# Kernel tuning notes

Measured on AMD Instinct MI355X. Metric: run time of the kernel, lower is better.

## Reference

```python
import jax, jax.numpy as jnp
import numpy as np

N, K, W = 500000, 512, 64


def setup_inputs() -> dict:
    key = jax.random.key(0)
    kx, kc = jax.random.split(key)
    X = jax.random.normal(kx, (N, W), dtype=jnp.float32)
    # nn.init.uniform_(codebook.weight, a=-1.0, b=1.0)
    codebook = jax.random.uniform(kc, (K, W), dtype=jnp.float32, minval=-1.0, maxval=1.0)
    return {"X": X, "codebook": codebook}


def reference(X, codebook):
    # torch.cdist (p=2): pairwise Euclidean distances [N, K]
    x2 = jnp.sum(X * X, axis=-1, keepdims=True)          # [N, 1]
    c2 = jnp.sum(codebook * codebook, axis=-1)           # [K]
    d2 = x2 - 2.0 * (X @ codebook.T) + c2[None, :]        # [N, K]
    dist = jnp.sqrt(jnp.maximum(d2, 0.0))
    idx = jnp.argmin(dist, axis=-1)                       # [N] int
    min_dists = jnp.min(dist, axis=-1)                    # [N] == gather(dist, idx)
    return idx, min_dists
```

## Files before the change

### kernel.cpp

```cpp
#include <hip/hip_runtime.h>

#define N_POINTS 500000
#define K_CENT   512
#define W_DIM    64
#define N_JOBS   (N_POINTS / 32)

typedef _Float16 half8 __attribute__((ext_vector_type(8)));
typedef float    f32x4 __attribute__((ext_vector_type(4)));

__global__ void cvt_kernel(const float* __restrict__ cb,
                           _Float16* __restrict__ cbf) {
    int id = blockIdx.x * 256 + threadIdx.x;
    if (id >= K_CENT * 8) return;
    int c = id >> 3, o = (id & 7) * 8;
    int t = c >> 5, csub = (c >> 4) & 1, r = c & 15;
    int kstep = o >> 5, grp = (o >> 3) & 3;
    int lane = grp * 16 + r;
    const float* src = cb + (size_t)c * W_DIM + o;
    half8 h, l;
#pragma unroll
    for (int j = 0; j < 8; ++j) {
        float w = -2.0f * src[j];
        _Float16 hh = (_Float16)w;
        h[j] = hh;
        l[j] = (_Float16)(w - (float)hh);
    }
    size_t bh = ((((size_t)t * 2 + 0) * 2 + csub) * 2 + kstep) * 512 + (size_t)lane * 8;
    size_t bl = ((((size_t)t * 2 + 1) * 2 + csub) * 2 + kstep) * 512 + (size_t)lane * 8;
    *(half8*)(cbf + bh) = h;
    *(half8*)(cbf + bl) = l;
}

__global__ void c2_kernel(const float* __restrict__ cb, float* __restrict__ c2) {
    int c = blockIdx.x * 256 + threadIdx.x;
    if (c >= K_CENT) return;
    const float4* row = (const float4*)(cb + (size_t)c * W_DIM);
    double s = 0.0;
#pragma unroll
    for (int j = 0; j < W_DIM / 4; ++j) {
        float4 v = row[j];
        s += (double)v.x * v.x + (double)v.y * v.y + (double)v.z * v.z + (double)v.w * v.w;
    }
    c2[c] = (float)s;
}

#define MFMA16(A, B, C) __builtin_amdgcn_mfma_f32_16x16x32_f16(A, B, C, 0, 0, 0)

#define STAGE(T, BUF)                                                          \
    {                                                                          \
        const __attribute__((address_space(1))) _Float16* g =                  \
            (const __attribute__((address_space(1))) _Float16*)                \
            (cbf + (size_t)(T) * 4096 + (size_t)wave * 1024 + (size_t)lane * 8); \
        __builtin_amdgcn_global_load_lds(                                      \
            (const __attribute__((address_space(1))) void*)g,                  \
            (__attribute__((address_space(3))) void*)&abuf[BUF][wave * 1024],  \
            16, 0, 0);                                                         \
        __builtin_amdgcn_global_load_lds(                                      \
            (const __attribute__((address_space(1))) void*)(g + 512),          \
            (__attribute__((address_space(3))) void*)&abuf[BUF][wave * 1024 + 512], \
            16, 0, 0);                                                         \
    }

#define MFMA_PHASE(BUF, ACC, Q0, Q1)                                           \
    {                                                                          \
        half8 aH[2][2], aL[2][2];                                              \
        _Pragma("unroll")                                                      \
        for (int cs = 0; cs < 2; ++cs)                                         \
            _Pragma("unroll")                                                  \
            for (int ks = 0; ks < 2; ++ks) {                                   \
                aH[cs][ks] = *(const half8*)&abuf[BUF][(cs * 2 + ks) * 512 + lane * 8]; \
                aL[cs][ks] = *(const half8*)&abuf[BUF][(4 + cs * 2 + ks) * 512 + lane * 8]; \
            }                                                                  \
        __builtin_amdgcn_s_setprio(1);                                         \
        _Pragma("unroll")                                                      \
        for (int cs = 0; cs < 2; ++cs)                                         \
            _Pragma("unroll")                                                  \
            for (int ps = 0; ps < 2; ++ps)                                     \
                ACC[cs][ps] = MFMA16(aH[cs][0], bh[ps][0], cs ? Q1 : Q0);      \
        _Pragma("unroll")                                                      \
        for (int cs = 0; cs < 2; ++cs)                                         \
            _Pragma("unroll")                                                  \
            for (int ps = 0; ps < 2; ++ps)                                     \
                ACC[cs][ps] = MFMA16(aH[cs][1], bh[ps][1], ACC[cs][ps]);       \
        _Pragma("unroll")                                                      \
        for (int cs = 0; cs < 2; ++cs)                                         \
            _Pragma("unroll")                                                  \
            for (int ps = 0; ps < 2; ++ps)                                     \
                ACC[cs][ps] = MFMA16(aL[cs][0], bh[ps][0], ACC[cs][ps]);       \
        _Pragma("unroll")                                                      \
        for (int cs = 0; cs < 2; ++cs)                                         \
            _Pragma("unroll")                                                  \
            for (int ps = 0; ps < 2; ++ps)                                     \
                ACC[cs][ps] = MFMA16(aL[cs][1], bh[ps][1], ACC[cs][ps]);       \
        _Pragma("unroll")                                                      \
        for (int cs = 0; cs < 2; ++cs)                                         \
            _Pragma("unroll")                                                  \
            for (int ps = 0; ps < 2; ++ps)                                     \
                ACC[cs][ps] = MFMA16(aH[cs][0], bl[ps][0], ACC[cs][ps]);       \
        _Pragma("unroll")                                                      \
        for (int cs = 0; cs < 2; ++cs)                                         \
            _Pragma("unroll")                                                  \
            for (int ps = 0; ps < 2; ++ps)                                     \
                ACC[cs][ps] = MFMA16(aH[cs][1], bl[ps][1], ACC[cs][ps]);       \
        __builtin_amdgcn_s_setprio(0);                                         \
    }

#define PAIR_ARGMIN(TA)                                                        \
    {                                                                          \
        _Pragma("unroll")                                                      \
        for (int ps = 0; ps < 2; ++ps) {                                       \
            float v0 = accP[0][ps][0], v1 = accP[0][ps][1];                    \
            float v2 = accP[0][ps][2], v3 = accP[0][ps][3];                    \
            float v4 = accP[1][ps][0], v5 = accP[1][ps][1];                    \
            float v6 = accP[1][ps][2], v7 = accP[1][ps][3];                    \
            float v8 = accQ[0][ps][0], v9 = accQ[0][ps][1];                    \
            float v10 = accQ[0][ps][2], v11 = accQ[0][ps][3];                  \
            float v12 = accQ[1][ps][0], v13 = accQ[1][ps][1];                  \
            float v14 = accQ[1][ps][2], v15 = accQ[1][ps][3];                  \
            float a0 = fminf(v0, v1),   a1 = fminf(v2, v3);                    \
            float a2 = fminf(v4, v5),   a3 = fminf(v6, v7);                    \
            float a4 = fminf(v8, v9),   a5 = fminf(v10, v11);                  \
            float a6 = fminf(v12, v13), a7 = fminf(v14, v15);                  \
            float b0 = fminf(a0, a1), b1 = fminf(a2, a3);                      \
            float b2 = fminf(a4, a5), b3 = fminf(a6, a7);                      \
            float c0 = fminf(b0, b1), c1 = fminf(b2, b3);                      \
            float m  = fminf(c0, c1);                                          \
            bool  L3 = (m == c0);                                              \
            float bL = L3 ? b0 : b2;                                           \
            bool  L2 = (m == bL);                                              \
            float aL = L3 ? (L2 ? a0 : a2) : (L2 ? a4 : a6);                   \
            bool  L1 = (m == aL);                                              \
            float vE = L3 ? (L2 ? (L1 ? v0 : v2) : (L1 ? v4 : v6))             \
                          : (L2 ? (L1 ? v8 : v10) : (L1 ? v12 : v14));         \
            bool  L0 = (m == vE);                                              \
            int ji = (L3 ? 0 : 8) | (L2 ? 0 : 4) | (L1 ? 0 : 2) | (L0 ? 0 : 1); \
            int jj = ji & 7;                                                   \
            int ci = ((TA) + (ji >> 3)) * 32 + (jj >> 2) * 16 + grp4 + (jj & 3); \
            bool imp = (m < bd[ps]) || (m == bd[ps] && ci < bi[ps]);           \
            bd[ps] = imp ? m : bd[ps];                                         \
            bi[ps] = imp ? ci : bi[ps];                                        \
        }                                                                      \
    }

__global__ __launch_bounds__(256, 2)
void kmeans_mfma(const float* __restrict__ X,
                 const _Float16* __restrict__ cbf,
                 const float* __restrict__ c2,
                 float* __restrict__ out_idx,
                 float* __restrict__ out_dist) {
    __shared__ _Float16 abuf[2][4096];
    __shared__ float c2s[K_CENT];
    int tid = threadIdx.x;
    c2s[tid] = c2[tid];
    c2s[tid + 256] = c2[tid + 256];

    int wave = tid >> 6;
    int lane = tid & 63;
    int l15  = lane & 15;
    int grp  = lane >> 4;
    int grp4 = grp * 4;
    int grp8 = grp * 8;
    int rot  = (blockIdx.x & 7) * 2;

    int job   = blockIdx.x * 4 + wave;
    int valid = job < N_JOBS;
    int jc    = valid ? job : (N_JOBS - 1);

    half8 bh[2][2], bl[2][2];
    float x2[2] = {0.f, 0.f};
#pragma unroll
    for (int ps = 0; ps < 2; ++ps) {
        int p = jc * 32 + ps * 16 + l15;
#pragma unroll
        for (int ks = 0; ks < 2; ++ks) {
            const float4* xp = (const float4*)(X + (size_t)p * W_DIM + ks * 32 + grp8);
            float4 f0 = xp[0], f1 = xp[1];
            float fa[8] = {f0.x, f0.y, f0.z, f0.w, f1.x, f1.y, f1.z, f1.w};
#pragma unroll
            for (int j = 0; j < 8; ++j) {
                _Float16 hh = (_Float16)fa[j];
                bh[ps][ks][j] = hh;
                bl[ps][ks][j] = (_Float16)(fa[j] - (float)hh);
                x2[ps] = fmaf(fa[j], fa[j], x2[ps]);
            }
        }
    }
#pragma unroll
    for (int ps = 0; ps < 2; ++ps) {
        x2[ps] += __shfl_xor(x2[ps], 16);
        x2[ps] += __shfl_xor(x2[ps], 32);
    }

    float bd[2] = {3.4e38f, 3.4e38f};
    int   bi[2] = {0, 0};
    f32x4 accP[2][2], accQ[2][2];

    STAGE(rot, 0)
    __syncthreads();

#pragma unroll 1
    for (int it = 0; it < 8; ++it) {
        int ta = (rot + 2 * it) & 15;
        f32x4 qa0 = *(const f32x4*)&c2s[ta * 32 + grp4];
        f32x4 qa1 = *(const f32x4*)&c2s[ta * 32 + 16 + grp4];
        f32x4 qb0 = *(const f32x4*)&c2s[ta * 32 + 32 + grp4];
        f32x4 qb1 = *(const f32x4*)&c2s[ta * 32 + 48 + grp4];
        STAGE(ta + 1, 1)
        MFMA_PHASE(0, accP, qa0, qa1)
        __syncthreads();
        if (it < 7) {
            int tn = (ta + 2) & 15;
            STAGE(tn, 0)
        }
        MFMA_PHASE(1, accQ, qb0, qb1)
        PAIR_ARGMIN(ta)
        __syncthreads();
    }

#pragma unroll
    for (int ps = 0; ps < 2; ++ps) {
        float od = __shfl_xor(bd[ps], 16); int oi = __shfl_xor(bi[ps], 16);
        if (od < bd[ps] || (od == bd[ps] && oi < bi[ps])) { bd[ps] = od; bi[ps] = oi; }
        od = __shfl_xor(bd[ps], 32); oi = __shfl_xor(bi[ps], 32);
        if (od < bd[ps] || (od == bd[ps] && oi < bi[ps])) { bd[ps] = od; bi[ps] = oi; }
    }

    if (valid && grp == 0) {
#pragma unroll
        for (int ps = 0; ps < 2; ++ps) {
            int p = jc * 32 + ps * 16 + l15;
            out_idx[p]  = (float)bi[ps];
            out_dist[p] = sqrtf(fmaxf(bd[ps] + x2[ps], 0.f));
        }
    }
}

extern "C" void kernel_launch(void* const* d_in, const int* in_sizes, int n_in,
                              void* d_out, int out_size, void* d_ws, size_t ws_size,
                              hipStream_t stream) {
    const float* X  = (const float*)d_in[0];
    const float* cb = (const float*)d_in[1];
    float* out      = (float*)d_out;

    _Float16* cbf = (_Float16*)d_ws;
    float*    c2  = (float*)(cbf + (size_t)K_CENT * W_DIM * 2);

    hipLaunchKernelGGL(cvt_kernel, dim3((K_CENT * 8 + 255) / 256), dim3(256), 0, stream, cb, cbf);
    hipLaunchKernelGGL(c2_kernel, dim3((K_CENT + 255) / 256), dim3(256), 0, stream, cb, c2);

    hipLaunchKernelGGL(kmeans_mfma, dim3((N_JOBS + 3) / 4), dim3(256), 0, stream,
                       X, cbf, c2, out, out + N_POINTS);
}
```

Before: 101.5 us.

## Process 64 points per wave to double codebook tile reuse

Each wave now handles 64 points (four 16-point groups) instead of 32, so every codebook tile staged in LDS is reused across twice as many MFMA columns. This halves the number of blocks and the total codebook staging and LDS reads per point. The argmin is done per 32-centroid chunk rather than per pair of chunks, and bounds guards handle the tail since 500000 is not divisible by 64. The cost is higher register pressure from the doubled accumulators and split-precision point fragments, which may reduce occupancy.

```diff
diff --git a/kernel.cpp b/kernel.cpp
--- a/kernel.cpp
+++ b/kernel.cpp
@@ -3,7 +3,7 @@
 #define N_POINTS 500000
 #define K_CENT   512
 #define W_DIM    64
-#define N_JOBS   (N_POINTS / 32)
+#define N_JOBS   ((N_POINTS + 63) / 64)
 
 typedef _Float16 half8 __attribute__((ext_vector_type(8)));
 typedef float    f32x4 __attribute__((ext_vector_type(4)));
@@ -61,7 +61,7 @@
             16, 0, 0);                                                         \
     }
 
-#define MFMA_PHASE(BUF, ACC, Q0, Q1)                                           \
+#define CHUNK_COMPUTE(BUF, T_)                                                 \
     {                                                                          \
         half8 aH[2][2], aL[2][2];                                              \
         _Pragma("unroll")                                                      \
@@ -71,71 +71,58 @@
                 aH[cs][ks] = *(const half8*)&abuf[BUF][(cs * 2 + ks) * 512 + lane * 8]; \
                 aL[cs][ks] = *(const half8*)&abuf[BUF][(4 + cs * 2 + ks) * 512 + lane * 8]; \
             }                                                                  \
+        f32x4 q0 = *(const f32x4*)&c2s[(T_) * 32 + grp4];                      \
+        f32x4 q1 = *(const f32x4*)&c2s[(T_) * 32 + 16 + grp4];                 \
+        f32x4 acc[2][4];                                                       \
         __builtin_amdgcn_s_setprio(1);                                         \
         _Pragma("unroll")                                                      \
         for (int cs = 0; cs < 2; ++cs)                                         \
             _Pragma("unroll")                                                  \
-            for (int ps = 0; ps < 2; ++ps)                                     \
-                ACC[cs][ps] = MFMA16(aH[cs][0], bh[ps][0], cs ? Q1 : Q0);      \
-        _Pragma("unroll")                                                      \
-        for (int cs = 0; cs < 2; ++cs)                                         \
-            _Pragma("unroll")                                                  \
-            for (int ps = 0; ps < 2; ++ps)                                     \
-                ACC[cs][ps] = MFMA16(aH[cs][1], bh[ps][1], ACC[cs][ps]);       \
-        _Pragma("unroll")                                                      \
-        for (int cs = 0; cs < 2; ++cs)                                         \
-            _Pragma("unroll")                                                  \
-            for (int ps = 0; ps < 2; ++ps)                                     \
-                ACC[cs][ps] = MFMA16(aL[cs][0], bh[ps][0], ACC[cs][ps]);       \
-        _Pragma("unroll")                                                      \
-        for (int cs = 0; cs < 2; ++cs)                                         \
-            _Pragma("unroll")                                                  \
-            for (int ps = 0; ps < 2; ++ps)                                     \
-                ACC[cs][ps] = MFMA16(aL[cs][1], bh[ps][1], ACC[cs][ps]);       \
-        _Pragma("unroll")                                                      \
-        for (int cs = 0; cs < 2; ++cs)                                         \
-            _Pragma("unroll")                                                  \
-            for (int ps = 0; ps < 2; ++ps)                                     \
-                ACC[cs][ps] = MFMA16(aH[cs][0], bl[ps][0], ACC[cs][ps]);       \
-        _Pragma("unroll")                                                      \
-        for (int cs = 0; cs < 2; ++cs)                                         \
-            _Pragma("unroll")                                                  \
-            for (int ps = 0; ps < 2; ++ps)                                     \
-                ACC[cs][ps] = MFMA16(aH[cs][1], bl[ps][1], ACC[cs][ps]);       \
+            for (int ps = 0; ps < 4; ++ps)                                     \
+                acc[cs][ps] = MFMA16(aH[cs][0], bh[ps][0], cs ? q1 : q0);      \
+        _Pragma("unroll")                                                      \
+        for (int cs = 0; cs < 2; ++cs)                                         \
+            _Pragma("unroll")                                                  \
+            for (int ps = 0; ps < 4; ++ps)                                     \
+                acc[cs][ps] = MFMA16(aH[cs][1], bh[ps][1], acc[cs][ps]);       \
+        _Pragma("unroll")                                                      \
+        for (int cs = 0; cs < 2; ++cs)                                         \
+            _Pragma("unroll")                                                  \
+            for (int ps = 0; ps < 4; ++ps)                                     \
+                acc[cs][ps] = MFMA16(aL[cs][0], bh[ps][0], acc[cs][ps]);       \
+        _Pragma("unroll")                                                      \
+        for (int cs = 0; cs < 2; ++cs)                                         \
+            _Pragma("unroll")                                                  \
+            for (int ps = 0; ps < 4; ++ps)                                     \
+                acc[cs][ps] = MFMA16(aL[cs][1], bh[ps][1], acc[cs][ps]);       \
+        _Pragma("unroll")                                                      \
+        for (int cs = 0; cs < 2; ++cs)                                         \
+            _Pragma("unroll")                                                  \
+            for (int ps = 0; ps < 4; ++ps)                                     \
+                acc[cs][ps] = MFMA16(aH[cs][0], bl[ps][0], acc[cs][ps]);       \
+        _Pragma("unroll")                                                      \
+        for (int cs = 0; cs < 2; ++cs)                                         \
+            _Pragma("unroll")                                                  \
+            for (int ps = 0; ps < 4; ++ps)                                     \
+                acc[cs][ps] = MFMA16(aH[cs][1], bl[ps][1], acc[cs][ps]);       \
         __builtin_amdgcn_s_setprio(0);                                         \
-    }
-
-#define PAIR_ARGMIN(TA)                                                        \
-    {                                                                          \
-        _Pragma("unroll")                                                      \
-        for (int ps = 0; ps < 2; ++ps) {                                       \
-            float v0 = accP[0][ps][0], v1 = accP[0][ps][1];                    \
-            float v2 = accP[0][ps][2], v3 = accP[0][ps][3];                    \
-            float v4 = accP[1][ps][0], v5 = accP[1][ps][1];                    \
-            float v6 = accP[1][ps][2], v7 = accP[1][ps][3];                    \
-            float v8 = accQ[0][ps][0], v9 = accQ[0][ps][1];                    \
-            float v10 = accQ[0][ps][2], v11 = accQ[0][ps][3];                  \
-            float v12 = accQ[1][ps][0], v13 = accQ[1][ps][1];                  \
-            float v14 = accQ[1][ps][2], v15 = accQ[1][ps][3];                  \
-            float a0 = fminf(v0, v1),   a1 = fminf(v2, v3);                    \
-            float a2 = fminf(v4, v5),   a3 = fminf(v6, v7);                    \
-            float a4 = fminf(v8, v9),   a5 = fminf(v10, v11);                  \
-            float a6 = fminf(v12, v13), a7 = fminf(v14, v15);                  \
+        _Pragma("unroll")                                                      \
+        for (int ps = 0; ps < 4; ++ps) {                                       \
+            float v0 = acc[0][ps][0], v1 = acc[0][ps][1];                      \
+            float v2 = acc[0][ps][2], v3 = acc[0][ps][3];                      \
+            float v4 = acc[1][ps][0], v5 = acc[1][ps][1];                      \
+            float v6 = acc[1][ps][2], v7 = acc[1][ps][3];                      \
+            float a0 = fminf(v0, v1), a1 = fminf(v2, v3);                      \
+            float a2 = fminf(v4, v5), a3 = fminf(v6, v7);                      \
             float b0 = fminf(a0, a1), b1 = fminf(a2, a3);                      \
-            float b2 = fminf(a4, a5), b3 = fminf(a6, a7);                      \
-            float c0 = fminf(b0, b1), c1 = fminf(b2, b3);                      \
-            float m  = fminf(c0, c1);                                          \
-            bool  L3 = (m == c0);                                              \
-            float bL = L3 ? b0 : b2;                                           \
-            bool  L2 = (m == bL);                                              \
-            float aL = L3 ? (L2 ? a0 : a2) : (L2 ? a4 : a6);                   \
-            bool  L1 = (m == aL);                                              \
-            float vE = L3 ? (L2 ? (L1 ? v0 : v2) : (L1 ? v4 : v6))             \
-                          : (L2 ? (L1 ? v8 : v10) : (L1 ? v12 : v14));         \
+            float m  = fminf(b0, b1);                                          \
+            bool  L2 = (m == b0);                                              \
+            float aLv = L2 ? a0 : a2;                                          \
+            bool  L1 = (m == aLv);                                             \
+            float vE = L2 ? (L1 ? v0 : v2) : (L1 ? v4 : v6);                   \
             bool  L0 = (m == vE);                                              \
-            int ji = (L3 ? 0 : 8) | (L2 ? 0 : 4) | (L1 ? 0 : 2) | (L0 ? 0 : 1); \
-            int jj = ji & 7;                                                   \
-            int ci = ((TA) + (ji >> 3)) * 32 + (jj >> 2) * 16 + grp4 + (jj & 3); \
+            int ji = (L2 ? 0 : 4) | (L1 ? 0 : 2) | (L0 ? 0 : 1);               \
+            int ci = (T_) * 32 + (ji >> 2) * 16 + grp4 + (ji & 3);             \
             bool imp = (m < bd[ps]) || (m == bd[ps] && ci < bi[ps]);           \
             bd[ps] = imp ? m : bd[ps];                                         \
             bi[ps] = imp ? ci : bi[ps];                                        \
@@ -166,14 +153,15 @@
     int valid = job < N_JOBS;
     int jc    = valid ? job : (N_JOBS - 1);
 
-    half8 bh[2][2], bl[2][2];
-    float x2[2] = {0.f, 0.f};
-#pragma unroll
-    for (int ps = 0; ps < 2; ++ps) {
-        int p = jc * 32 + ps * 16 + l15;
+    half8 bh[4][2], bl[4][2];
+    float x2[4] = {0.f, 0.f, 0.f, 0.f};
+#pragma unroll
+    for (int ps = 0; ps < 4; ++ps) {
+        int p  = jc * 64 + ps * 16 + l15;
+        int pe = p < N_POINTS ? p : (N_POINTS - 1);
 #pragma unroll
         for (int ks = 0; ks < 2; ++ks) {
-            const float4* xp = (const float4*)(X + (size_t)p * W_DIM + ks * 32 + grp8);
+            const float4* xp = (const float4*)(X + (size_t)pe * W_DIM + ks * 32 + grp8);
             float4 f0 = xp[0], f1 = xp[1];
             float fa[8] = {f0.x, f0.y, f0.z, f0.w, f1.x, f1.y, f1.z, f1.w};
 #pragma unroll
@@ -186,14 +174,13 @@
         }
     }
 #pragma unroll
-    for (int ps = 0; ps < 2; ++ps) {
+    for (int ps = 0; ps < 4; ++ps) {
         x2[ps] += __shfl_xor(x2[ps], 16);
         x2[ps] += __shfl_xor(x2[ps], 32);
     }
 
-    float bd[2] = {3.4e38f, 3.4e38f};
-    int   bi[2] = {0, 0};
-    f32x4 accP[2][2], accQ[2][2];
+    float bd[4] = {3.4e38f, 3.4e38f, 3.4e38f, 3.4e38f};
+    int   bi[4] = {0, 0, 0, 0};
 
     STAGE(rot, 0)
     __syncthreads();
@@ -201,24 +188,19 @@
 #pragma unroll 1
     for (int it = 0; it < 8; ++it) {
         int ta = (rot + 2 * it) & 15;
-        f32x4 qa0 = *(const f32x4*)&c2s[ta * 32 + grp4];
-        f32x4 qa1 = *(const f32x4*)&c2s[ta * 32 + 16 + grp4];
-        f32x4 qb0 = *(const f32x4*)&c2s[ta * 32 + 32 + grp4];
-        f32x4 qb1 = *(const f32x4*)&c2s[ta * 32 + 48 + grp4];
         STAGE(ta + 1, 1)
-        MFMA_PHASE(0, accP, qa0, qa1)
+        CHUNK_COMPUTE(0, ta)
         __syncthreads();
         if (it < 7) {
             int tn = (ta + 2) & 15;
             STAGE(tn, 0)
         }
-        MFMA_PHASE(1, accQ, qb0, qb1)
-        PAIR_ARGMIN(ta)
+        CHUNK_COMPUTE(1, ta + 1)
         __syncthreads();
     }
 
 #pragma unroll
-    for (int ps = 0; ps < 2; ++ps) {
+    for (int ps = 0; ps < 4; ++ps) {
         float od = __shfl_xor(bd[ps], 16); int oi = __shfl_xor(bi[ps], 16);
         if (od < bd[ps] || (od == bd[ps] && oi < bi[ps])) { bd[ps] = od; bi[ps] = oi; }
         od = __shfl_xor(bd[ps], 32); oi = __shfl_xor(bi[ps], 32);
@@ -227,10 +209,12 @@
 
     if (valid && grp == 0) {
 #pragma unroll
-        for (int ps = 0; ps < 2; ++ps) {
-            int p = jc * 32 + ps * 16 + l15;
-            out_idx[p]  = (float)bi[ps];
-            out_dist[p] = sqrtf(fmaxf(bd[ps] + x2[ps], 0.f));
+        for (int ps = 0; ps < 4; ++ps) {
+            int p = jc * 64 + ps * 16 + l15;
+            if (p < N_POINTS) {
+                out_idx[p]  = (float)bi[ps];
+                out_dist[p] = sqrtf(fmaxf(bd[ps] + x2[ps], 0.f));
+            }
         }
     }
 }
```

Result: slower. 105.3 us (+3.7%).

## Stage centroid tile pairs per buffer to halve barriers per iteration

Applied to the files above, without the earlier changes.

Each double-buffer slot now holds two consecutive centroid tiles instead of one, and each wave issues four global-to-LDS loads per stage. The prefetch of the next pair is issued at the top of the iteration into the other buffer. Both MFMA phases then run on the current buffer with a single barrier per iteration. This removes one __syncthreads per iteration and gives loads a full iteration to land, at the cost of doubling the LDS buffer (about 34 KB per block), which could pressure occupancy.

```diff
diff --git a/kernel.cpp b/kernel.cpp
--- a/kernel.cpp
+++ b/kernel.cpp
@@ -46,30 +46,34 @@
 
 #define MFMA16(A, B, C) __builtin_amdgcn_mfma_f32_16x16x32_f16(A, B, C, 0, 0, 0)
 
-#define STAGE(T, BUF)                                                          \
+#define STAGE_PAIR(T, BUF)                                                     \
     {                                                                          \
         const __attribute__((address_space(1))) _Float16* g =                  \
             (const __attribute__((address_space(1))) _Float16*)                \
-            (cbf + (size_t)(T) * 4096 + (size_t)wave * 1024 + (size_t)lane * 8); \
+            (cbf + (size_t)(T) * 4096 + (size_t)wave * 2048 + (size_t)lane * 8); \
         __builtin_amdgcn_global_load_lds(                                      \
             (const __attribute__((address_space(1))) void*)g,                  \
-            (__attribute__((address_space(3))) void*)&abuf[BUF][wave * 1024],  \
-            16, 0, 0);                                                         \
+            (__attribute__((address_space(3))) void*)&abuf[BUF][wave * 2048], 16, 0, 0); \
         __builtin_amdgcn_global_load_lds(                                      \
             (const __attribute__((address_space(1))) void*)(g + 512),          \
-            (__attribute__((address_space(3))) void*)&abuf[BUF][wave * 1024 + 512], \
-            16, 0, 0);                                                         \
-    }
-
-#define MFMA_PHASE(BUF, ACC, Q0, Q1)                                           \
+            (__attribute__((address_space(3))) void*)&abuf[BUF][wave * 2048 + 512], 16, 0, 0); \
+        __builtin_amdgcn_global_load_lds(                                      \
+            (const __attribute__((address_space(1))) void*)(g + 1024),         \
+            (__attribute__((address_space(3))) void*)&abuf[BUF][wave * 2048 + 1024], 16, 0, 0); \
+        __builtin_amdgcn_global_load_lds(                                      \
+            (const __attribute__((address_space(1))) void*)(g + 1536),         \
+            (__attribute__((address_space(3))) void*)&abuf[BUF][wave * 2048 + 1536], 16, 0, 0); \
+    }
+
+#define MFMA_PHASE(BUF, OFF, ACC, Q0, Q1)                                      \
     {                                                                          \
         half8 aH[2][2], aL[2][2];                                              \
         _Pragma("unroll")                                                      \
         for (int cs = 0; cs < 2; ++cs)                                         \
             _Pragma("unroll")                                                  \
             for (int ks = 0; ks < 2; ++ks) {                                   \
-                aH[cs][ks] = *(const half8*)&abuf[BUF][(cs * 2 + ks) * 512 + lane * 8]; \
-                aL[cs][ks] = *(const half8*)&abuf[BUF][(4 + cs * 2 + ks) * 512 + lane * 8]; \
+                aH[cs][ks] = *(const half8*)&abuf[BUF][(OFF) + (cs * 2 + ks) * 512 + lane * 8]; \
+                aL[cs][ks] = *(const half8*)&abuf[BUF][(OFF) + 2048 + (cs * 2 + ks) * 512 + lane * 8]; \
             }                                                                  \
         __builtin_amdgcn_s_setprio(1);                                         \
         _Pragma("unroll")                                                      \
@@ -148,7 +152,7 @@
                  const float* __restrict__ c2,
                  float* __restrict__ out_idx,
                  float* __restrict__ out_dist) {
-    __shared__ _Float16 abuf[2][4096];
+    __shared__ _Float16 abuf[2][8192];
     __shared__ float c2s[K_CENT];
     int tid = threadIdx.x;
     c2s[tid] = c2[tid];
@@ -195,24 +199,23 @@
     int   bi[2] = {0, 0};
     f32x4 accP[2][2], accQ[2][2];
 
-    STAGE(rot, 0)
+    STAGE_PAIR(rot, 0)
     __syncthreads();
 
 #pragma unroll 1
     for (int it = 0; it < 8; ++it) {
         int ta = (rot + 2 * it) & 15;
+        int b  = it & 1;
+        if (it < 7) {
+            int tn = (ta + 2) & 15;
+            STAGE_PAIR(tn, b ^ 1)
+        }
         f32x4 qa0 = *(const f32x4*)&c2s[ta * 32 + grp4];
         f32x4 qa1 = *(const f32x4*)&c2s[ta * 32 + 16 + grp4];
         f32x4 qb0 = *(const f32x4*)&c2s[ta * 32 + 32 + grp4];
         f32x4 qb1 = *(const f32x4*)&c2s[ta * 32 + 48 + grp4];
-        STAGE(ta + 1, 1)
-        MFMA_PHASE(0, accP, qa0, qa1)
-        __syncthreads();
-        if (it < 7) {
-            int tn = (ta + 2) & 15;
-            STAGE(tn, 0)
-        }
-        MFMA_PHASE(1, accQ, qb0, qb1)
+        MFMA_PHASE(b, 0,    accP, qa0, qa1)
+        MFMA_PHASE(b, 4096, accQ, qb0, qb1)
         PAIR_ARGMIN(ta)
         __syncthreads();
     }
```

Measured after the change: 100.7 us, median of 3. No clear change (-0.8%).

## Keep codebook slices register-resident per wave and stream point tiles through LDS

Applied to the files above, without the earlier changes.

Swaps which operand stays stationary. Each of 8 waves now holds its 64-centroid slice of the codebook (hi/lo fp16 split) plus the matching c2 values in registers for the whole kernel. Persistent-style blocks of 512 threads walk 62 point tiles each, staging every 32-point tile into LDS as hi/lo fp16 with x2 computed by the block. Per-wave partial argmins are merged across waves through shared memory, one tile behind the compute, which removes the repeated per-block codebook streaming and c2 staging. In exchange it adds more barriers per tile, a cross-wave reduction step, heavier register pressure, and a grid of only about 252 blocks.

```diff
diff --git a/kernel.cpp b/kernel.cpp
--- a/kernel.cpp
+++ b/kernel.cpp
@@ -1,11 +1,14 @@
 #include <hip/hip_runtime.h>
 
-#define N_POINTS 500000
-#define K_CENT   512
-#define W_DIM    64
-#define N_JOBS   (N_POINTS / 32)
+#define N_POINTS  500000
+#define K_CENT    512
+#define W_DIM     64
+#define N_TILES   (N_POINTS / 32)
+#define TPB_TILES 62
+#define N_BLOCKS  ((N_TILES + TPB_TILES - 1) / TPB_TILES)
 
 typedef _Float16 half8 __attribute__((ext_vector_type(8)));
+typedef _Float16 half4 __attribute__((ext_vector_type(4)));
 typedef float    f32x4 __attribute__((ext_vector_type(4)));
 
 __global__ void cvt_kernel(const float* __restrict__ cb,
@@ -46,77 +49,93 @@
 
 #define MFMA16(A, B, C) __builtin_amdgcn_mfma_f32_16x16x32_f16(A, B, C, 0, 0, 0)
 
-#define STAGE(T, BUF)                                                          \
+#define STAGE(T)                                                               \
     {                                                                          \
-        const __attribute__((address_space(1))) _Float16* g =                  \
-            (const __attribute__((address_space(1))) _Float16*)                \
-            (cbf + (size_t)(T) * 4096 + (size_t)wave * 1024 + (size_t)lane * 8); \
-        __builtin_amdgcn_global_load_lds(                                      \
-            (const __attribute__((address_space(1))) void*)g,                  \
-            (__attribute__((address_space(3))) void*)&abuf[BUF][wave * 1024],  \
-            16, 0, 0);                                                         \
-        __builtin_amdgcn_global_load_lds(                                      \
-            (const __attribute__((address_space(1))) void*)(g + 512),          \
-            (__attribute__((address_space(3))) void*)&abuf[BUF][wave * 1024 + 512], \
-            16, 0, 0);                                                         \
-    }
-
-#define MFMA_PHASE(BUF, ACC, Q0, Q1)                                           \
+        int p  = tid >> 4, dq = tid & 15, d = dq * 4;                          \
+        const float4 f = *(const float4*)(X + ((size_t)(T) * 32 + p) * W_DIM + d); \
+        half4 hi, lo;                                                          \
+        hi[0] = (_Float16)f.x; lo[0] = (_Float16)(f.x - (float)hi[0]);         \
+        hi[1] = (_Float16)f.y; lo[1] = (_Float16)(f.y - (float)hi[1]);         \
+        hi[2] = (_Float16)f.z; lo[2] = (_Float16)(f.z - (float)hi[2]);         \
+        hi[3] = (_Float16)f.w; lo[3] = (_Float16)(f.w - (float)hi[3]);         \
+        float x2p = f.x * f.x + f.y * f.y + f.z * f.z + f.w * f.w;             \
+        x2p += __shfl_xor(x2p, 1);                                             \
+        x2p += __shfl_xor(x2p, 2);                                             \
+        x2p += __shfl_xor(x2p, 4);                                             \
+        x2p += __shfl_xor(x2p, 8);                                             \
+        if (dq == 0) x2buf[(T) % 3][p] = x2p;                                  \
+        int ps = p >> 4, lp = p & 15, ks = d >> 5, gd = (d >> 3) & 3, j0 = d & 7; \
+        int ls = gd * 16 + lp;                                                 \
+        *(half4*)&Bbuf[(T) & 1][((ps * 2 + 0) * 2 + ks) * 512 + ls * 8 + j0] = hi; \
+        *(half4*)&Bbuf[(T) & 1][((ps * 2 + 1) * 2 + ks) * 512 + ls * 8 + j0] = lo; \
+    }
+
+#define COMPUTE(T)                                                             \
     {                                                                          \
-        half8 aH[2][2], aL[2][2];                                              \
-        _Pragma("unroll")                                                      \
-        for (int cs = 0; cs < 2; ++cs)                                         \
+        int buf_ = (T) & 1;                                                    \
+        half8 bh[2][2], bl[2][2];                                              \
+        _Pragma("unroll")                                                      \
+        for (int ps = 0; ps < 2; ++ps)                                         \
             _Pragma("unroll")                                                  \
             for (int ks = 0; ks < 2; ++ks) {                                   \
-                aH[cs][ks] = *(const half8*)&abuf[BUF][(cs * 2 + ks) * 512 + lane * 8]; \
-                aL[cs][ks] = *(const half8*)&abuf[BUF][(4 + cs * 2 + ks) * 512 + lane * 8]; \
+                bh[ps][ks] = *(const half8*)&Bbuf[buf_][((ps * 2 + 0) * 2 + ks) * 512 + lane * 8]; \
+                bl[ps][ks] = *(const half8*)&Bbuf[buf_][((ps * 2 + 1) * 2 + ks) * 512 + lane * 8]; \
             }                                                                  \
+        f32x4 acc[2][2][2];                                                    \
         __builtin_amdgcn_s_setprio(1);                                         \
         _Pragma("unroll")                                                      \
-        for (int cs = 0; cs < 2; ++cs)                                         \
-            _Pragma("unroll")                                                  \
-            for (int ps = 0; ps < 2; ++ps)                                     \
-                ACC[cs][ps] = MFMA16(aH[cs][0], bh[ps][0], cs ? Q1 : Q0);      \
-        _Pragma("unroll")                                                      \
-        for (int cs = 0; cs < 2; ++cs)                                         \
-            _Pragma("unroll")                                                  \
-            for (int ps = 0; ps < 2; ++ps)                                     \
-                ACC[cs][ps] = MFMA16(aH[cs][1], bh[ps][1], ACC[cs][ps]);       \
-        _Pragma("unroll")                                                      \
-        for (int cs = 0; cs < 2; ++cs)                                         \
-            _Pragma("unroll")                                                  \
-            for (int ps = 0; ps < 2; ++ps)                                     \
-                ACC[cs][ps] = MFMA16(aL[cs][0], bh[ps][0], ACC[cs][ps]);       \
-        _Pragma("unroll")                                                      \
-        for (int cs = 0; cs < 2; ++cs)                                         \
-            _Pragma("unroll")                                                  \
-            for (int ps = 0; ps < 2; ++ps)                                     \
-                ACC[cs][ps] = MFMA16(aL[cs][1], bh[ps][1], ACC[cs][ps]);       \
-        _Pragma("unroll")                                                      \
-        for (int cs = 0; cs < 2; ++cs)                                         \
-            _Pragma("unroll")                                                  \
-            for (int ps = 0; ps < 2; ++ps)                                     \
-                ACC[cs][ps] = MFMA16(aH[cs][0], bl[ps][0], ACC[cs][ps]);       \
-        _Pragma("unroll")                                                      \
-        for (int cs = 0; cs < 2; ++cs)                                         \
-            _Pragma("unroll")                                                  \
-            for (int ps = 0; ps < 2; ++ps)                                     \
-                ACC[cs][ps] = MFMA16(aH[cs][1], bl[ps][1], ACC[cs][ps]);       \
+        for (int c = 0; c < 2; ++c)                                            \
+            _Pragma("unroll")                                                  \
+            for (int cs = 0; cs < 2; ++cs)                                     \
+                _Pragma("unroll")                                              \
+                for (int ps = 0; ps < 2; ++ps)                                 \
+                    acc[c][cs][ps] = MFMA16(aH[c][cs][0], bh[ps][0], q[c][cs]); \
+        _Pragma("unroll")                                                      \
+        for (int c = 0; c < 2; ++c)                                            \
+            _Pragma("unroll")                                                  \
+            for (int cs = 0; cs < 2; ++cs)                                     \
+                _Pragma("unroll")                                              \
+                for (int ps = 0; ps < 2; ++ps)                                 \
+                    acc[c][cs][ps] = MFMA16(aH[c][cs][1], bh[ps][1], acc[c][cs][ps]); \
+        _Pragma("unroll")                                                      \
+        for (int c = 0; c < 2; ++c)                                            \
+            _Pragma("unroll")                                                  \
+            for (int cs = 0; cs < 2; ++cs)                                     \
+                _Pragma("unroll")                                              \
+                for (int ps = 0; ps < 2; ++ps)                                 \
+                    acc[c][cs][ps] = MFMA16(aL[c][cs][0], bh[ps][0], acc[c][cs][ps]); \
+        _Pragma("unroll")                                                      \
+        for (int c = 0; c < 2; ++c)                                            \
+            _Pragma("unroll")                                                  \
+            for (int cs = 0; cs < 2; ++cs)                                     \
+                _Pragma("unroll")                                              \
+                for (int ps = 0; ps < 2; ++ps)                                 \
+                    acc[c][cs][ps] = MFMA16(aL[c][cs][1], bh[ps][1], acc[c][cs][ps]); \
+        _Pragma("unroll")                                                      \
+        for (int c = 0; c < 2; ++c)                                            \
+            _Pragma("unroll")                                                  \
+            for (int cs = 0; cs < 2; ++cs)                                     \
+                _Pragma("unroll")                                              \
+                for (int ps = 0; ps < 2; ++ps)                                 \
+                    acc[c][cs][ps] = MFMA16(aH[c][cs][0], bl[ps][0], acc[c][cs][ps]); \
+        _Pragma("unroll")                                                      \
+        for (int c = 0; c < 2; ++c)                                            \
+            _Pragma("unroll")                                                  \
+            for (int cs = 0; cs < 2; ++cs)                                     \
+                _Pragma("unroll")                                              \
+                for (int ps = 0; ps < 2; ++ps)                                 \
+                    acc[c][cs][ps] = MFMA16(aH[c][cs][1], bl[ps][1], acc[c][cs][ps]); \
         __builtin_amdgcn_s_setprio(0);                                         \
-    }
-
-#define PAIR_ARGMIN(TA)                                                        \
-    {                                                                          \
         _Pragma("unroll")                                                      \
         for (int ps = 0; ps < 2; ++ps) {                                       \
-            float v0 = accP[0][ps][0], v1 = accP[0][ps][1];                    \
-            float v2 = accP[0][ps][2], v3 = accP[0][ps][3];                    \
-            float v4 = accP[1][ps][0], v5 = accP[1][ps][1];                    \
-            float v6 = accP[1][ps][2], v7 = accP[1][ps][3];                    \
-            float v8 = accQ[0][ps][0], v9 = accQ[0][ps][1];                    \
-            float v10 = accQ[0][ps][2], v11 = accQ[0][ps][3];                  \
-            float v12 = accQ[1][ps][0], v13 = accQ[1][ps][1];                  \
-            float v14 = accQ[1][ps][2], v15 = accQ[1][ps][3];                  \
+            float v0 = acc[0][0][ps][0], v1 = acc[0][0][ps][1];                \
+            float v2 = acc[0][0][ps][2], v3 = acc[0][0][ps][3];                \
+            float v4 = acc[0][1][ps][0], v5 = acc[0][1][ps][1];                \
+            float v6 = acc[0][1][ps][2], v7 = acc[0][1][ps][3];                \
+            float v8 = acc[1][0][ps][0], v9 = acc[1][0][ps][1];                \
+            float v10 = acc[1][0][ps][2], v11 = acc[1][0][ps][3];              \
+            float v12 = acc[1][1][ps][0], v13 = acc[1][1][ps][1];              \
+            float v14 = acc[1][1][ps][2], v15 = acc[1][1][ps][3];              \
             float a0 = fminf(v0, v1),   a1 = fminf(v2, v3);                    \
             float a2 = fminf(v4, v5),   a3 = fminf(v6, v7);                    \
             float a4 = fminf(v8, v9),   a5 = fminf(v10, v11);                  \
@@ -128,111 +147,96 @@
             bool  L3 = (m == c0);                                              \
             float bL = L3 ? b0 : b2;                                           \
             bool  L2 = (m == bL);                                              \
-            float aL = L3 ? (L2 ? a0 : a2) : (L2 ? a4 : a6);                   \
-            bool  L1 = (m == aL);                                              \
+            float aLv = L3 ? (L2 ? a0 : a2) : (L2 ? a4 : a6);                  \
+            bool  L1 = (m == aLv);                                             \
             float vE = L3 ? (L2 ? (L1 ? v0 : v2) : (L1 ? v4 : v6))             \
                           : (L2 ? (L1 ? v8 : v10) : (L1 ? v12 : v14));         \
             bool  L0 = (m == vE);                                              \
             int ji = (L3 ? 0 : 8) | (L2 ? 0 : 4) | (L1 ? 0 : 2) | (L0 ? 0 : 1); \
-            int jj = ji & 7;                                                   \
-            int ci = ((TA) + (ji >> 3)) * 32 + (jj >> 2) * 16 + grp4 + (jj & 3); \
-            bool imp = (m < bd[ps]) || (m == bd[ps] && ci < bi[ps]);           \
-            bd[ps] = imp ? m : bd[ps];                                         \
-            bi[ps] = imp ? ci : bi[ps];                                        \
+            int ci = wb + (ji >> 3) * 32 + ((ji >> 2) & 1) * 16 + grp4 + (ji & 3); \
+            float bdp = m; int bip = ci;                                       \
+            float od = __shfl_xor(bdp, 16); int oi = __shfl_xor(bip, 16);      \
+            if (od < bdp || (od == bdp && oi < bip)) { bdp = od; bip = oi; }   \
+            od = __shfl_xor(bdp, 32); oi = __shfl_xor(bip, 32);                \
+            if (od < bdp || (od == bdp && oi < bip)) { bdp = od; bip = oi; }   \
+            if (grp == 0) {                                                    \
+                partd[buf_][wave][ps * 16 + l15] = bdp;                        \
+                parti[buf_][wave][ps * 16 + l15] = (float)bip;                 \
+            }                                                                  \
         }                                                                      \
     }
 
-__global__ __launch_bounds__(256, 2)
+#define COMBINE(T)                                                             \
+    {                                                                          \
+        if (tid < 32) {                                                        \
+            int buf_ = (T) & 1;                                                \
+            int p = tid;                                                       \
+            float bdv = partd[buf_][0][p];                                     \
+            float biv = parti[buf_][0][p];                                     \
+            _Pragma("unroll")                                                  \
+            for (int w = 1; w < 8; ++w) {                                      \
+                float od = partd[buf_][w][p], oi = parti[buf_][w][p];          \
+                bool imp = (od < bdv) || (od == bdv && oi < biv);              \
+                bdv = imp ? od : bdv;                                          \
+                biv = imp ? oi : biv;                                          \
+            }                                                                  \
+            float x2v = x2buf[(T) % 3][p];                                     \
+            size_t pp = (size_t)(T) * 32 + p;                                  \
+            out_idx[pp]  = biv;                                                \
+            out_dist[pp] = sqrtf(fmaxf(bdv + x2v, 0.f));                       \
+        }                                                                      \
+    }
+
+__global__ __launch_bounds__(512, 2)
 void kmeans_mfma(const float* __restrict__ X,
                  const _Float16* __restrict__ cbf,
                  const float* __restrict__ c2,
                  float* __restrict__ out_idx,
                  float* __restrict__ out_dist) {
-    __shared__ _Float16 abuf[2][4096];
-    __shared__ float c2s[K_CENT];
-    int tid = threadIdx.x;
-    c2s[tid] = c2[tid];
-    c2s[tid + 256] = c2[tid + 256];
-
+    __shared__ _Float16 Bbuf[2][4096];
+    __shared__ float partd[2][8][32];
+    __shared__ float parti[2][8][32];
+    __shared__ float x2buf[3][32];
+
+    int tid  = threadIdx.x;
     int wave = tid >> 6;
     int lane = tid & 63;
     int l15  = lane & 15;
     int grp  = lane >> 4;
     int grp4 = grp * 4;
-    int grp8 = grp * 8;
-    int rot  = (blockIdx.x & 7) * 2;
-
-    int job   = blockIdx.x * 4 + wave;
-    int valid = job < N_JOBS;
-    int jc    = valid ? job : (N_JOBS - 1);
-
-    half8 bh[2][2], bl[2][2];
-    float x2[2] = {0.f, 0.f};
-#pragma unroll
-    for (int ps = 0; ps < 2; ++ps) {
-        int p = jc * 32 + ps * 16 + l15;
-#pragma unroll
-        for (int ks = 0; ks < 2; ++ks) {
-            const float4* xp = (const float4*)(X + (size_t)p * W_DIM + ks * 32 + grp8);
-            float4 f0 = xp[0], f1 = xp[1];
-            float fa[8] = {f0.x, f0.y, f0.z, f0.w, f1.x, f1.y, f1.z, f1.w};
-#pragma unroll
-            for (int j = 0; j < 8; ++j) {
-                _Float16 hh = (_Float16)fa[j];
-                bh[ps][ks][j] = hh;
-                bl[ps][ks][j] = (_Float16)(fa[j] - (float)hh);
-                x2[ps] = fmaf(fa[j], fa[j], x2[ps]);
+    int wb   = wave * 64;
+
+    half8 aH[2][2][2], aL[2][2][2];
+    f32x4 q[2][2];
+#pragma unroll
+    for (int c = 0; c < 2; ++c) {
+#pragma unroll
+        for (int cs = 0; cs < 2; ++cs) {
+#pragma unroll
+            for (int ks = 0; ks < 2; ++ks) {
+                size_t bh_ = ((((size_t)(2 * wave + c) * 2 + 0) * 2 + cs) * 2 + ks) * 512 + (size_t)lane * 8;
+                size_t bl_ = ((((size_t)(2 * wave + c) * 2 + 1) * 2 + cs) * 2 + ks) * 512 + (size_t)lane * 8;
+                aH[c][cs][ks] = *(const half8*)(cbf + bh_);
+                aL[c][cs][ks] = *(const half8*)(cbf + bl_);
             }
+            q[c][cs] = *(const f32x4*)(c2 + wb + c * 32 + cs * 16 + grp4);
         }
     }
-#pragma unroll
-    for (int ps = 0; ps < 2; ++ps) {
-        x2[ps] += __shfl_xor(x2[ps], 16);
-        x2[ps] += __shfl_xor(x2[ps], 32);
-    }
-
-    float bd[2] = {3.4e38f, 3.4e38f};
-    int   bi[2] = {0, 0};
-    f32x4 accP[2][2], accQ[2][2];
-
-    STAGE(rot, 0)
+
+    int t0 = blockIdx.x * TPB_TILES;
+    int t1 = t0 + TPB_TILES; if (t1 > N_TILES) t1 = N_TILES;
+
+    STAGE(t0)
     __syncthreads();
 
 #pragma unroll 1
-    for (int it = 0; it < 8; ++it) {
-        int ta = (rot + 2 * it) & 15;
-        f32x4 qa0 = *(const f32x4*)&c2s[ta * 32 + grp4];
-        f32x4 qa1 = *(const f32x4*)&c2s[ta * 32 + 16 + grp4];
-        f32x4 qb0 = *(const f32x4*)&c2s[ta * 32 + 32 + grp4];
-        f32x4 qb1 = *(const f32x4*)&c2s[ta * 32 + 48 + grp4];
-        STAGE(ta + 1, 1)
-        MFMA_PHASE(0, accP, qa0, qa1)
+    for (int t = t0; t < t1; ++t) {
+        if (t + 1 < t1) STAGE(t + 1)
+        COMPUTE(t)
+        if (t > t0) COMBINE(t - 1)
         __syncthreads();
-        if (it < 7) {
-            int tn = (ta + 2) & 15;
-            STAGE(tn, 0)
-        }
-        MFMA_PHASE(1, accQ, qb0, qb1)
-        PAIR_ARGMIN(ta)
-        __syncthreads();
-    }
-
-#pragma unroll
-    for (int ps = 0; ps < 2; ++ps) {
-        float od = __shfl_xor(bd[ps], 16); int oi = __shfl_xor(bi[ps], 16);
-        if (od < bd[ps] || (od == bd[ps] && oi < bi[ps])) { bd[ps] = od; bi[ps] = oi; }
-        od = __shfl_xor(bd[ps], 32); oi = __shfl_xor(bi[ps], 32);
-        if (od < bd[ps] || (od == bd[ps] && oi < bi[ps])) { bd[ps] = od; bi[ps] = oi; }
-    }
-
-    if (valid && grp == 0) {
-#pragma unroll
-        for (int ps = 0; ps < 2; ++ps) {
-            int p = jc * 32 + ps * 16 + l15;
-            out_idx[p]  = (float)bi[ps];
-            out_dist[p] = sqrtf(fmaxf(bd[ps] + x2[ps], 0.f));
-        }
-    }
+    }
+    COMBINE(t1 - 1)
 }
 
 extern "C" void kernel_launch(void* const* d_in, const int* in_sizes, int n_in,
@@ -248,6 +252,6 @@
     hipLaunchKernelGGL(cvt_kernel, dim3((K_CENT * 8 + 255) / 256), dim3(256), 0, stream, cb, cbf);
     hipLaunchKernelGGL(c2_kernel, dim3((K_CENT + 255) / 256), dim3(256), 0, stream, cb, c2);
 
-    hipLaunchKernelGGL(kmeans_mfma, dim3((N_JOBS + 3) / 4), dim3(256), 0, stream,
+    hipLaunchKernelGGL(kmeans_mfma, dim3(N_BLOCKS), dim3(512), 0, stream,
                        X, cbf, c2, out, out + N_POINTS);
 }
```

Measured after the change: 152.1 us. 49.9% more time.
